# Kernel tuning notes

Measured on AMD Instinct MI355X. Metric: run time of the kernel, lower is better.

## Reference

```python
import jax, jax.numpy as jnp
import numpy as np

B, N, DIM = 4, 2048, 1024
HEADS, DIM_HEAD = 16, 64
INNER = HEADS * DIM_HEAD
SCALE = DIM_HEAD ** -0.5


def setup_inputs() -> dict:
    key = jax.random.key(0)
    k1, k2, k3 = jax.random.split(key, 3)
    x = jax.random.normal(k1, (B, N, DIM), dtype=jnp.float32)
    w_qkv = jax.random.normal(k2, (DIM, 3 * INNER), dtype=jnp.float32) * (DIM ** -0.5)
    w_out = jax.random.normal(k3, (INNER, DIM), dtype=jnp.float32) * (INNER ** -0.5)
    b_out = jnp.zeros((DIM,), dtype=jnp.float32)
    return {"x": x, "w_qkv": w_qkv, "w_out": w_out, "b_out": b_out}


def reference(x, w_qkv, w_out, b_out):
    # qkv projection: [B, N, 3*inner]
    qkv = jnp.einsum('bnd,de->bne', x, w_qkv)
    q, k, v = jnp.split(qkv, 3, axis=-1)
    # 'b n (h d) -> b h n d'
    split_heads = lambda t: t.reshape(B, N, HEADS, DIM_HEAD).transpose(0, 2, 1, 3)
    q, k, v = split_heads(q), split_heads(k), split_heads(v)
    dots = jnp.einsum('bhid,bhjd->bhij', q, k) * SCALE  # [B, H, N, N]
    attn = jax.nn.softmax(dots, axis=-1)
    out = jnp.einsum('bhij,bhjd->bhid', attn, v)
    # 'b h n d -> b n (h d)'
    out = out.transpose(0, 2, 1, 3).reshape(B, N, INNER)
    out = jnp.einsum('bne,ed->bnd', out, w_out) + b_out
    return out
```

## Files before the change

### kernel.cpp

```cpp
#include <hip/hip_runtime.h>
#include <hip/hip_bf16.h>
#include <stdint.h>

typedef float f32x4 __attribute__((ext_vector_type(4)));
typedef float f32x16 __attribute__((ext_vector_type(16)));
typedef short s16x8 __attribute__((ext_vector_type(8)));
typedef unsigned u32x4 __attribute__((ext_vector_type(4)));
typedef unsigned short us16;

#define LOG2E 1.44269504088896340736f

__device__ __forceinline__ us16 f2b(float f) {
  union { float f; unsigned u; } v; v.f = f;
  return (us16)((v.u + 0x7fffu + ((v.u >> 16) & 1u)) >> 16);
}

__device__ __forceinline__ unsigned cvtpk(float lo, float hi) {
  unsigned r;
  asm("v_cvt_pk_bf16_f32 %0, %1, %2" : "=v"(r) : "v"(lo), "v"(hi));
  return r;
}

__device__ __forceinline__ void plswap(unsigned& a, unsigned& b) {
  asm volatile("v_permlane32_swap_b32 %0, %1" : "+v"(a), "+v"(b));
}

__device__ __forceinline__ void gload16(const void* g, void* l) {
  __builtin_amdgcn_global_load_lds((__attribute__((address_space(1))) void*)g,
                                   (__attribute__((address_space(3))) void*)l,
                                   16, 0, 0);
}

#define MFMA16(acc, a, b) \
  (acc) = __builtin_amdgcn_mfma_f32_16x16x32_bf16((a), (b), (acc), 0, 0, 0)
#define MFMA32(acc, a, b) \
  (acc) = __builtin_amdgcn_mfma_f32_32x32x16_bf16((a), (b), (acc), 0, 0, 0)

__global__ void convx_kernel(const float* __restrict__ x, us16* __restrict__ xb) {
  const int idx = blockIdx.x * 256 + threadIdx.x;
  const float4 v = ((const float4*)x)[idx];
  ushort4 o;
  o.x = f2b(v.x); o.y = f2b(v.y); o.z = f2b(v.z); o.w = f2b(v.w);
  ((ushort4*)xb)[idx] = o;
}

__global__ void convw_kernel(const float* __restrict__ wqkv, const float* __restrict__ wout,
                             us16* __restrict__ wqkvT, us16* __restrict__ woutT) {
  __shared__ float tile[64][65];
  const int bid = blockIdx.x;
  const bool isq = bid < 768;
  const int j = isq ? bid : bid - 768;
  const int ntiles = isq ? 48 : 16;
  const int nt = j % ntiles, kt = j / ntiles;
  const int NN = isq ? 3072 : 1024;
  const float* W = isq ? wqkv : wout;
  us16* WT = isq ? wqkvT : woutT;
  const int n0 = nt * 64, k0 = kt * 64;
  const int t = threadIdx.x;
  const int tc = t & 63, tr = t >> 6;
#pragma unroll
  for (int p = 0; p < 16; ++p)
    tile[p * 4 + tr][tc] = W[(size_t)(k0 + p * 4 + tr) * NN + n0 + tc];
  __syncthreads();
#pragma unroll
  for (int p = 0; p < 16; ++p) {
    const int nl = p * 4 + tr;
    float v = tile[tc][nl];
    if (isq && (n0 + nl) < 1024) v *= 0.125f * LOG2E;
    WT[(size_t)(n0 + nl) * 1024 + k0 + tc] = f2b(v);
  }
}

__global__ __launch_bounds__(512, 2)
void gemm8p(const us16* __restrict__ A, const us16* __restrict__ Bm,
            us16* __restrict__ C) {
  __shared__ us16 As[2][2][128 * 64];
  __shared__ us16 Bs[2][2][128 * 64];
  const int t = threadIdx.x;
  const int l = t & 63;
  const int lr = l & 15, lh = l >> 4;
  const int w = t >> 6;
  const int wm = w >> 2, wn = w & 3;

  const int bid = blockIdx.x;
  const int swz = (bid & 7) * 48 + (bid >> 3);
  const size_t m0 = (size_t)(swz & 31) * 256;
  const size_t n0 = (size_t)(swz >> 5) * 256;

  f32x4 acc[8][4] = {};

  auto stage = [&](us16* dst, const us16* src, size_t rb, int kt2) {
    if (kt2 < 16) {
#pragma unroll
      for (int i2 = 0; i2 < 2; ++i2) {
        const int e = i2 * 512 + t;
        const int row = e >> 3, slot = e & 7;
        gload16(src + (rb + row) * 1024 + kt2 * 64 + ((slot ^ (row & 7)) << 3),
                dst + e * 8);
      }
    }
  };

  stage(&As[0][0][0], A, m0, 0);        stage(&As[0][1][0], A, m0 + 128, 0);
  stage(&Bs[0][0][0], Bm, n0, 0);       stage(&Bs[0][1][0], Bm, n0 + 128, 0);
  stage(&Bs[1][0][0], Bm, n0, 1);       stage(&Bs[1][1][0], Bm, n0 + 128, 1);
  asm volatile("s_waitcnt vmcnt(0)" ::: "memory");
  asm volatile("s_barrier" ::: "memory");

  const us16* aL = &As[0][wm][0];
  const us16* aH = &As[1][wm][0];
  const us16* bL = &Bs[0][wn >> 1][0];
  const us16* bH = &Bs[1][wn >> 1][0];
  const int brow0 = (wn & 1) * 64;

  for (int it = 0; it < 8; ++it) {
    const int T = 2 * it;
    s16x8 bv[4][2];
#pragma unroll
    for (int p = 0; p < 8; ++p) {
      const int q = p & 3;
      const us16* ab = (p < 4) ? aL : aH;
      const us16* bb = (p < 4) ? bL : bH;
      s16x8 av[2][2];
#pragma unroll
      for (int j = 0; j < 2; ++j)
#pragma unroll
        for (int ks = 0; ks < 2; ++ks) {
          const int row = (2 * q + j) * 16 + lr;
          const int slot = (ks * 4 + lh) ^ (lr & 7);
          av[j][ks] = *(const s16x8*)&ab[row * 64 + slot * 8];
        }
      if (q == 0) {
#pragma unroll
        for (int fc = 0; fc < 4; ++fc)
#pragma unroll
          for (int ks = 0; ks < 2; ++ks) {
            const int row = brow0 + fc * 16 + lr;
            const int slot = (ks * 4 + lh) ^ (lr & 7);
            bv[fc][ks] = *(const s16x8*)&bb[row * 64 + slot * 8];
          }
      }
      switch (p) {
        case 0: stage(&As[1][0][0], A, m0, T + 1); break;
        case 1: stage(&As[1][1][0], A, m0 + 128, T + 1); break;
        case 2: stage(&Bs[0][0][0], Bm, n0, T + 2); break;
        case 3: stage(&Bs[0][1][0], Bm, n0 + 128, T + 2); break;
        case 4: stage(&As[0][0][0], A, m0, T + 2); break;
        case 5: stage(&As[0][1][0], A, m0 + 128, T + 2); break;
        case 6: stage(&Bs[1][0][0], Bm, n0, T + 3); break;
        case 7: stage(&Bs[1][1][0], Bm, n0 + 128, T + 3); break;
      }
      asm volatile("s_barrier" ::: "memory");
      __builtin_amdgcn_s_setprio(1);
#pragma unroll
      for (int fc = 0; fc < 4; ++fc)
#pragma unroll
        for (int j = 0; j < 2; ++j)
#pragma unroll
          for (int ks = 0; ks < 2; ++ks)
            MFMA16(acc[2 * q + j][fc], av[j][ks], bv[fc][ks]);
      __builtin_amdgcn_s_setprio(0);
      if (p == 3 || p == 7) {
        if (it == 7) { asm volatile("s_waitcnt vmcnt(0)" ::: "memory"); }
        else         { asm volatile("s_waitcnt vmcnt(4)" ::: "memory"); }
      }
      asm volatile("s_barrier" ::: "memory");
    }
  }
#pragma unroll
  for (int fr = 0; fr < 8; ++fr) {
    const size_t r0 = m0 + wm * 128 + fr * 16 + lh * 4;
#pragma unroll
    for (int fc = 0; fc < 4; ++fc) {
      const size_t col = n0 + wn * 64 + fc * 16 + lr;
#pragma unroll
      for (int rg = 0; rg < 4; ++rg)
        C[(r0 + rg) * 3072 + col] = f2b(acc[fr][fc][rg]);
    }
  }
}

template <int OUT_BF16>
__global__ __launch_bounds__(256, 2)
void gemm_bt(const us16* __restrict__ A, const us16* __restrict__ B,
             void* __restrict__ C, const float* __restrict__ bias, int N) {
  __shared__ us16 sm[2][2][128 * 64];
  const int t = threadIdx.x;
  const int l = t & 63;
  const int lr = l & 15, lh = l >> 4;
  const int w = t >> 6;
  const int wm = w >> 1, wn = w & 1;
  const int bm = blockIdx.x & 63;
  const int bn = blockIdx.x >> 6;
  const size_t m0 = (size_t)bm * 128, n0 = (size_t)bn * 128;

  f32x4 acc[4][4] = {};

  auto stage = [&](int buf, int kt) {
    const int k0 = kt << 6;
#pragma unroll
    for (int i = 0; i < 4; ++i) {
      const int e = i * 256 + t;
      const int r = e >> 3, c = (e & 7) << 3;
      gload16(A + (m0 + r) * 1024 + k0 + c, &sm[buf][0][e * 8]);
      gload16(B + (n0 + r) * 1024 + k0 + c, &sm[buf][1][e * 8]);
    }
  };

  stage(0, 0);
  __syncthreads();
  int cur = 0;
  for (int kt = 0; kt < 16; ++kt) {
    if (kt < 15) stage(cur ^ 1, kt + 1);
    const us16* sA = &sm[cur][0][0];
    const us16* sB = &sm[cur][1][0];
#pragma unroll
    for (int kk = 0; kk < 64; kk += 32) {
      s16x8 av[4], bv[4];
#pragma unroll
      for (int i = 0; i < 4; ++i)
        av[i] = *(const s16x8*)&sA[(wm * 64 + i * 16 + lr) * 64 + kk + lh * 8];
#pragma unroll
      for (int jj = 0; jj < 4; ++jj)
        bv[jj] = *(const s16x8*)&sB[(wn * 64 + jj * 16 + lr) * 64 + kk + lh * 8];
#pragma unroll
      for (int i = 0; i < 4; ++i)
#pragma unroll
        for (int jj = 0; jj < 4; ++jj)
          MFMA16(acc[i][jj], av[i], bv[jj]);
    }
    __syncthreads();
    cur ^= 1;
  }
#pragma unroll
  for (int i = 0; i < 4; ++i) {
    const size_t row0 = m0 + wm * 64 + i * 16 + lh * 4;
#pragma unroll
    for (int jj = 0; jj < 4; ++jj) {
      const size_t col = n0 + wn * 64 + jj * 16 + lr;
#pragma unroll
      for (int r = 0; r < 4; ++r) {
        const float v = acc[i][jj][r];
        if constexpr (OUT_BF16) {
          ((us16*)C)[(row0 + r) * N + col] = f2b(v);
        } else {
          ((float*)C)[(row0 + r) * N + col] = v + bias[col];
        }
      }
    }
  }
}

__global__ __launch_bounds__(512)
void attn_kernel(const us16* __restrict__ qkv, us16* __restrict__ attno) {
  __shared__ us16 Klds[2][64 * 64];
  __shared__ us16 Vt[2][64 * 64];
  const int tid = threadIdx.x;
  const int l31 = tid & 31;
  const int hi = (tid >> 5) & 1;
  const int w = tid >> 6;

  const int bid = blockIdx.x;
  const int bh = (bid & 7) * 8 + (bid >> 5);
  const int qt = (bid >> 3) & 3;
  const int b = bh >> 4, h = bh & 15;

  const size_t rowbase = (size_t)b * 2048;
  const int kcol = 1024 + h * 64, vcol = 2048 + h * 64;
  const size_t qrow0 = rowbase + qt * 512 + w * 64;

  s16x8 qa[4], qb[4];
  {
    const us16* qpa = qkv + (qrow0 + l31) * 3072 + h * 64 + hi * 8;
    const us16* qpb = qkv + (qrow0 + 32 + l31) * 3072 + h * 64 + hi * 8;
#pragma unroll
    for (int s = 0; s < 4; ++s) {
      qa[s] = *(const s16x8*)(qpa + s * 16);
      qb[s] = *(const s16x8*)(qpb + s * 16);
    }
  }

  s16x8 ones;
#pragma unroll
  for (int i = 0; i < 8; ++i) ones[i] = (short)0x3F80;

  const int tid4 = tid - 256;
  const int kvv = (tid & 31) * 2;
  const int vd0 = ((tid >> 5) & 7) * 8;
  auto stageK = [&](int buf, int kt2) {
#pragma unroll
    for (int i = 0; i < 2; ++i) {
      const int e = i * 256 + tid4;
      const int kv = e >> 3, sl = e & 7;
      gload16(qkv + (rowbase + (size_t)kt2 * 64 + kv) * 3072 + kcol + ((sl ^ (kv & 7)) << 3),
              &Klds[buf][e * 8]);
    }
  };
  auto vload = [&](int kt2, s16x8& a, s16x8& c) {
    const us16* vp = qkv + (rowbase + (size_t)kt2 * 64 + kvv) * 3072 + vcol + vd0;
    a = *(const s16x8*)vp;
    c = *(const s16x8*)(vp + 3072);
  };
  auto vwrite = [&](int buf, const s16x8 a, const s16x8 c) {
#pragma unroll
    for (int i = 0; i < 8; ++i) {
      const int row = vd0 + i;
      const unsigned pk = (unsigned)(us16)a[i] | ((unsigned)(us16)c[i] << 16);
      *(unsigned*)&Vt[buf][row * 64 + (kvv ^ ((row & 7) << 3))] = pk;
    }
  };

  f32x16 oA0 = {}, oA1 = {}, oB0 = {}, oB1 = {};
  f32x16 lsA = {}, lsB = {};

  s16x8 vna, vnc;
  if (w < 4) { vload(0, vna, vnc); vwrite(0, vna, vnc); }
  else stageK(0, 0);
  __syncthreads();

  for (int kt = 0; kt < 32; ++kt) {
    const int cur = kt & 1;
    if (kt < 31) {
      if (w < 4) vload(kt + 1, vna, vnc);
      else stageK(cur ^ 1, kt + 1);
    }

    const us16* Kb = &Klds[cur][0];
    s16x8 kf0, kf1, kf2, kf3, kf4, kf5, kf6, kf7;
    {
      const int x7 = l31 & 7;
      kf0 = *(const s16x8*)&Kb[l31 * 64 + (((0 + hi) ^ x7) << 3)];
      kf1 = *(const s16x8*)&Kb[(32 + l31) * 64 + (((0 + hi) ^ x7) << 3)];
      kf2 = *(const s16x8*)&Kb[l31 * 64 + (((2 + hi) ^ x7) << 3)];
      kf3 = *(const s16x8*)&Kb[(32 + l31) * 64 + (((2 + hi) ^ x7) << 3)];
      kf4 = *(const s16x8*)&Kb[l31 * 64 + (((4 + hi) ^ x7) << 3)];
      kf5 = *(const s16x8*)&Kb[(32 + l31) * 64 + (((4 + hi) ^ x7) << 3)];
      kf6 = *(const s16x8*)&Kb[l31 * 64 + (((6 + hi) ^ x7) << 3)];
      kf7 = *(const s16x8*)&Kb[(32 + l31) * 64 + (((6 + hi) ^ x7) << 3)];
    }

    s16x8 paA[4], paB[4];
    {
      f32x16 st0 = {}, st1 = {};
      __builtin_amdgcn_s_setprio(1);
      MFMA32(st0, kf0, qa[0]); MFMA32(st1, kf1, qa[0]);
      MFMA32(st0, kf2, qa[1]); MFMA32(st1, kf3, qa[1]);
      MFMA32(st0, kf4, qa[2]); MFMA32(st1, kf5, qa[2]);
      MFMA32(st0, kf6, qa[3]); MFMA32(st1, kf7, qa[3]);
      __builtin_amdgcn_s_setprio(0);
#pragma unroll
      for (int r = 0; r < 16; ++r) {
        st0[r] = __builtin_amdgcn_exp2f(st0[r]);
        st1[r] = __builtin_amdgcn_exp2f(st1[r]);
      }
#pragma unroll
      for (int half = 0; half < 2; ++half) {
        const f32x16& sp = half ? st1 : st0;
#pragma unroll
        for (int g = 0; g < 2; ++g) {
          unsigned a0 = cvtpk(sp[8 * g + 0], sp[8 * g + 1]);
          unsigned a1 = cvtpk(sp[8 * g + 2], sp[8 * g + 3]);
          unsigned b0 = cvtpk(sp[8 * g + 4], sp[8 * g + 5]);
          unsigned b1 = cvtpk(sp[8 * g + 6], sp[8 * g + 7]);
          plswap(a0, b0);
          plswap(a1, b1);
          union { u32x4 u; s16x8 s; } cv;
          cv.u = (u32x4){a0, a1, b0, b1};
          paA[2 * half + g] = cv.s;
        }
      }
    }
    {
      f32x16 st0 = {}, st1 = {};
      __builtin_amdgcn_s_setprio(1);
      MFMA32(st0, kf0, qb[0]); MFMA32(st1, kf1, qb[0]);
      MFMA32(st0, kf2, qb[1]); MFMA32(st1, kf3, qb[1]);
      MFMA32(st0, kf4, qb[2]); MFMA32(st1, kf5, qb[2]);
      MFMA32(st0, kf6, qb[3]); MFMA32(st1, kf7, qb[3]);
      __builtin_amdgcn_s_setprio(0);
#pragma unroll
      for (int r = 0; r < 16; ++r) {
        st0[r] = __builtin_amdgcn_exp2f(st0[r]);
        st1[r] = __builtin_amdgcn_exp2f(st1[r]);
      }
#pragma unroll
      for (int half = 0; half < 2; ++half) {
        const f32x16& sp = half ? st1 : st0;
#pragma unroll
        for (int g = 0; g < 2; ++g) {
          unsigned a0 = cvtpk(sp[8 * g + 0], sp[8 * g + 1]);
          unsigned a1 = cvtpk(sp[8 * g + 2], sp[8 * g + 3]);
          unsigned b0 = cvtpk(sp[8 * g + 4], sp[8 * g + 5]);
          unsigned b1 = cvtpk(sp[8 * g + 6], sp[8 * g + 7]);
          plswap(a0, b0);
          plswap(a1, b1);
          union { u32x4 u; s16x8 s; } cv;
          cv.u = (u32x4){a0, a1, b0, b1};
          paB[2 * half + g] = cv.s;
        }
      }
    }

    const us16* Vb = &Vt[cur][0];
    __builtin_amdgcn_s_setprio(1);
#pragma unroll
    for (int ks = 0; ks < 4; ++ks) {
      const int sl = ((2 * ks + hi) ^ (l31 & 7)) << 3;
      const s16x8 vb0 = *(const s16x8*)&Vb[l31 * 64 + sl];
      const s16x8 vb1 = *(const s16x8*)&Vb[(32 + l31) * 64 + sl];
      MFMA32(oA0, paA[ks], vb0); MFMA32(oA1, paA[ks], vb1);
      MFMA32(oB0, paB[ks], vb0); MFMA32(oB1, paB[ks], vb1);
      MFMA32(lsA, paA[ks], ones); MFMA32(lsB, paB[ks], ones);
    }
    __builtin_amdgcn_s_setprio(0);

    if (kt < 31 && w < 4) vwrite(cur ^ 1, vna, vnc);
    __syncthreads();
  }

#pragma unroll
  for (int r = 0; r < 16; ++r) {
    const int q = (r & 3) + 8 * (r >> 2) + 4 * hi;
    const float fA = 1.0f / lsA[r];
    const float fB = 1.0f / lsB[r];
    const size_t rowA = qrow0 + q;
    const size_t rowB = qrow0 + 32 + q;
    attno[rowA * 1024 + h * 64 + l31] = f2b(oA0[r] * fA);
    attno[rowA * 1024 + h * 64 + 32 + l31] = f2b(oA1[r] * fA);
    attno[rowB * 1024 + h * 64 + l31] = f2b(oB0[r] * fB);
    attno[rowB * 1024 + h * 64 + 32 + l31] = f2b(oB1[r] * fB);
  }
}

extern "C" void kernel_launch(void* const* d_in, const int* in_sizes, int n_in,
                              void* d_out, int out_size, void* d_ws, size_t ws_size,
                              hipStream_t stream) {
  (void)in_sizes; (void)n_in; (void)out_size;
  const float* x     = (const float*)d_in[0];
  const float* w_qkv = (const float*)d_in[1];
  const float* w_out = (const float*)d_in[2];
  const float* b_out = (const float*)d_in[3];

  if (ws_size < 92274688u) return;
  char* ws = (char*)d_ws;
  us16* xb    = (us16*)(ws);
  us16* wqkvT = (us16*)(ws + 16777216);
  us16* woutT = (us16*)(ws + 23068672);
  us16* qkv   = (us16*)(ws + 25165824);
  us16* attno = (us16*)(ws + 75497472);

  convx_kernel<<<8192, 256, 0, stream>>>(x, xb);
  convw_kernel<<<1024, 256, 0, stream>>>(w_qkv, w_out, wqkvT, woutT);
  gemm8p<<<384, 512, 0, stream>>>(xb, wqkvT, qkv);
  attn_kernel<<<256, 512, 0, stream>>>(qkv, attno);
  gemm_bt<0><<<512, 256, 0, stream>>>(attno, woutT, d_out, b_out, 1024);
}
```

Before: 205.2 us.

## Shrink QKV GEMM tile to 256x128 and compute softmax row sums with VALU

The QKV projection GEMM now uses 256x128 output tiles with a 4x2 wave layout and twice as many blocks. This halves the B staging and accumulator registers and gives more blocks to spread across CUs. In exchange, each block reuses the A tile across fewer columns. The attention kernel drops the extra MFMAs against a ones vector that built the softmax denominators. It now sums the exponentials on the VALU per lane and combines them with a cross-lane shuffle before normalising, which removes matrix-core work but adds VALU adds and shuffles.

```diff
diff --git a/kernel.cpp b/kernel.cpp
--- a/kernel.cpp
+++ b/kernel.cpp
@@ -75,19 +75,19 @@
 void gemm8p(const us16* __restrict__ A, const us16* __restrict__ Bm,
             us16* __restrict__ C) {
   __shared__ us16 As[2][2][128 * 64];
-  __shared__ us16 Bs[2][2][128 * 64];
+  __shared__ us16 Bs[2][128 * 64];
   const int t = threadIdx.x;
   const int l = t & 63;
   const int lr = l & 15, lh = l >> 4;
   const int w = t >> 6;
-  const int wm = w >> 2, wn = w & 3;
+  const int wm = w >> 1, wn = w & 1;
 
   const int bid = blockIdx.x;
-  const int swz = (bid & 7) * 48 + (bid >> 3);
+  const int swz = (bid & 7) * 96 + (bid >> 3);
   const size_t m0 = (size_t)(swz & 31) * 256;
-  const size_t n0 = (size_t)(swz >> 5) * 256;
-
-  f32x4 acc[8][4] = {};
+  const size_t n0 = (size_t)(swz >> 5) * 128;
+
+  f32x4 acc[4][4] = {};
 
   auto stage = [&](us16* dst, const us16* src, size_t rb, int kt2) {
     if (kt2 < 16) {
@@ -101,34 +101,34 @@
     }
   };
 
-  stage(&As[0][0][0], A, m0, 0);        stage(&As[0][1][0], A, m0 + 128, 0);
-  stage(&Bs[0][0][0], Bm, n0, 0);       stage(&Bs[0][1][0], Bm, n0 + 128, 0);
-  stage(&Bs[1][0][0], Bm, n0, 1);       stage(&Bs[1][1][0], Bm, n0 + 128, 1);
+  stage(&As[0][0][0], A, m0, 0);
+  stage(&As[0][1][0], A, m0 + 128, 0);
+  stage(&Bs[0][0], Bm, n0, 0);
+  stage(&Bs[1][0], Bm, n0, 1);
   asm volatile("s_waitcnt vmcnt(0)" ::: "memory");
   asm volatile("s_barrier" ::: "memory");
 
-  const us16* aL = &As[0][wm][0];
-  const us16* aH = &As[1][wm][0];
-  const us16* bL = &Bs[0][wn >> 1][0];
-  const us16* bH = &Bs[1][wn >> 1][0];
-  const int brow0 = (wn & 1) * 64;
+  const int ahalf = wm >> 1;
+  const int arow0 = (wm & 1) * 64;
+  const int brow0 = wn * 64;
 
   for (int it = 0; it < 8; ++it) {
     const int T = 2 * it;
     s16x8 bv[4][2];
 #pragma unroll
-    for (int p = 0; p < 8; ++p) {
-      const int q = p & 3;
-      const us16* ab = (p < 4) ? aL : aH;
-      const us16* bb = (p < 4) ? bL : bH;
+    for (int p = 0; p < 4; ++p) {
+      const int tb = p >> 1;
+      const int q = p & 1;
+      const us16* aP = &As[tb][ahalf][0];
+      const us16* bP = &Bs[tb][0];
       s16x8 av[2][2];
 #pragma unroll
       for (int j = 0; j < 2; ++j)
 #pragma unroll
         for (int ks = 0; ks < 2; ++ks) {
-          const int row = (2 * q + j) * 16 + lr;
+          const int row = arow0 + (2 * q + j) * 16 + lr;
           const int slot = (ks * 4 + lh) ^ (lr & 7);
-          av[j][ks] = *(const s16x8*)&ab[row * 64 + slot * 8];
+          av[j][ks] = *(const s16x8*)&aP[row * 64 + slot * 8];
         }
       if (q == 0) {
 #pragma unroll
@@ -137,18 +137,16 @@
           for (int ks = 0; ks < 2; ++ks) {
             const int row = brow0 + fc * 16 + lr;
             const int slot = (ks * 4 + lh) ^ (lr & 7);
-            bv[fc][ks] = *(const s16x8*)&bb[row * 64 + slot * 8];
+            bv[fc][ks] = *(const s16x8*)&bP[row * 64 + slot * 8];
           }
       }
       switch (p) {
-        case 0: stage(&As[1][0][0], A, m0, T + 1); break;
-        case 1: stage(&As[1][1][0], A, m0 + 128, T + 1); break;
-        case 2: stage(&Bs[0][0][0], Bm, n0, T + 2); break;
-        case 3: stage(&Bs[0][1][0], Bm, n0 + 128, T + 2); break;
-        case 4: stage(&As[0][0][0], A, m0, T + 2); break;
-        case 5: stage(&As[0][1][0], A, m0 + 128, T + 2); break;
-        case 6: stage(&Bs[1][0][0], Bm, n0, T + 3); break;
-        case 7: stage(&Bs[1][1][0], Bm, n0 + 128, T + 3); break;
+        case 0: stage(&As[1][0][0], A, m0, T + 1);
+                stage(&As[1][1][0], A, m0 + 128, T + 1); break;
+        case 1: stage(&Bs[0][0], Bm, n0, T + 2); break;
+        case 2: stage(&As[0][0][0], A, m0, T + 2);
+                stage(&As[0][1][0], A, m0 + 128, T + 2); break;
+        case 3: stage(&Bs[1][0], Bm, n0, T + 3); break;
       }
       asm volatile("s_barrier" ::: "memory");
       __builtin_amdgcn_s_setprio(1);
@@ -160,16 +158,16 @@
           for (int ks = 0; ks < 2; ++ks)
             MFMA16(acc[2 * q + j][fc], av[j][ks], bv[fc][ks]);
       __builtin_amdgcn_s_setprio(0);
-      if (p == 3 || p == 7) {
+      if (p == 1 || p == 3) {
         if (it == 7) { asm volatile("s_waitcnt vmcnt(0)" ::: "memory"); }
-        else         { asm volatile("s_waitcnt vmcnt(4)" ::: "memory"); }
+        else         { asm volatile("s_waitcnt vmcnt(2)" ::: "memory"); }
       }
       asm volatile("s_barrier" ::: "memory");
     }
   }
 #pragma unroll
-  for (int fr = 0; fr < 8; ++fr) {
-    const size_t r0 = m0 + wm * 128 + fr * 16 + lh * 4;
+  for (int fr = 0; fr < 4; ++fr) {
+    const size_t r0 = m0 + wm * 64 + fr * 16 + lh * 4;
 #pragma unroll
     for (int fc = 0; fc < 4; ++fc) {
       const size_t col = n0 + wn * 64 + fc * 16 + lr;
@@ -280,10 +278,6 @@
     }
   }
 
-  s16x8 ones;
-#pragma unroll
-  for (int i = 0; i < 8; ++i) ones[i] = (short)0x3F80;
-
   const int tid4 = tid - 256;
   const int kvv = (tid & 31) * 2;
   const int vd0 = ((tid >> 5) & 7) * 8;
@@ -311,7 +305,7 @@
   };
 
   f32x16 oA0 = {}, oA1 = {}, oB0 = {}, oB1 = {};
-  f32x16 lsA = {}, lsB = {};
+  float lsA = 0.0f, lsB = 0.0f;
 
   s16x8 vna, vnc;
   if (w < 4) { vload(0, vna, vnc); vwrite(0, vna, vnc); }
@@ -348,11 +342,14 @@
       MFMA32(st0, kf4, qa[2]); MFMA32(st1, kf5, qa[2]);
       MFMA32(st0, kf6, qa[3]); MFMA32(st1, kf7, qa[3]);
       __builtin_amdgcn_s_setprio(0);
+      float ps = 0.0f;
 #pragma unroll
       for (int r = 0; r < 16; ++r) {
         st0[r] = __builtin_amdgcn_exp2f(st0[r]);
         st1[r] = __builtin_amdgcn_exp2f(st1[r]);
-      }
+        ps += st0[r] + st1[r];
+      }
+      lsA += ps;
 #pragma unroll
       for (int half = 0; half < 2; ++half) {
         const f32x16& sp = half ? st1 : st0;
@@ -378,11 +375,14 @@
       MFMA32(st0, kf4, qb[2]); MFMA32(st1, kf5, qb[2]);
       MFMA32(st0, kf6, qb[3]); MFMA32(st1, kf7, qb[3]);
       __builtin_amdgcn_s_setprio(0);
+      float ps = 0.0f;
 #pragma unroll
       for (int r = 0; r < 16; ++r) {
         st0[r] = __builtin_amdgcn_exp2f(st0[r]);
         st1[r] = __builtin_amdgcn_exp2f(st1[r]);
-      }
+        ps += st0[r] + st1[r];
+      }
+      lsB += ps;
 #pragma unroll
       for (int half = 0; half < 2; ++half) {
         const f32x16& sp = half ? st1 : st0;
@@ -410,7 +410,6 @@
       const s16x8 vb1 = *(const s16x8*)&Vb[(32 + l31) * 64 + sl];
       MFMA32(oA0, paA[ks], vb0); MFMA32(oA1, paA[ks], vb1);
       MFMA32(oB0, paB[ks], vb0); MFMA32(oB1, paB[ks], vb1);
-      MFMA32(lsA, paA[ks], ones); MFMA32(lsB, paB[ks], ones);
     }
     __builtin_amdgcn_s_setprio(0);
 
@@ -418,11 +417,14 @@
     __syncthreads();
   }
 
+  const float lA = lsA + __shfl_xor(lsA, 32);
+  const float lB = lsB + __shfl_xor(lsB, 32);
+  const float liA = 1.0f / lA, liB = 1.0f / lB;
 #pragma unroll
   for (int r = 0; r < 16; ++r) {
     const int q = (r & 3) + 8 * (r >> 2) + 4 * hi;
-    const float fA = 1.0f / lsA[r];
-    const float fB = 1.0f / lsB[r];
+    const float fA = __shfl(liA, q);
+    const float fB = __shfl(liB, q);
     const size_t rowA = qrow0 + q;
     const size_t rowB = qrow0 + 32 + q;
     attno[rowA * 1024 + h * 64 + l31] = f2b(oA0[r] * fA);
@@ -451,7 +453,7 @@
 
   convx_kernel<<<8192, 256, 0, stream>>>(x, xb);
   convw_kernel<<<1024, 256, 0, stream>>>(w_qkv, w_out, wqkvT, woutT);
-  gemm8p<<<384, 512, 0, stream>>>(xb, wqkvT, qkv);
+  gemm8p<<<768, 512, 0, stream>>>(xb, wqkvT, qkv);
   attn_kernel<<<256, 512, 0, stream>>>(qkv, attno);
   gemm_bt<0><<<512, 256, 0, stream>>>(attno, woutT, d_out, b_out, 1024);
 }
```

New measurement: 199.1 us. 3.0% less time.
